# Performance work log

Measured on AMD Instinct MI355X. Metric: run time of the kernel, lower is better.

The kernel has to match this reference:

```python
import jax, jax.numpy as jnp
import numpy as np

# Standard SMPL kinematic tree (child -> parent); root's entry unused.
PARENTS = np.array([0, 0, 0, 0, 1, 2, 3, 4, 5, 6, 7, 8, 9, 9, 9, 12, 13, 14, 16, 17, 18, 19, 20, 21], dtype=np.int32)
N_JOINTS = 24


def _rodrigues(r):
    # r: [..., 3] axis-angle -> [..., 3, 3] rotation matrices.
    # Original adds N(0,1e-8) noise to avoid div-by-zero; we use a deterministic eps.
    theta = jnp.linalg.norm(r, axis=-1, keepdims=True) + 1e-8
    rh = r / theta
    cos = jnp.cos(theta)[..., None]
    sin = jnp.sin(theta)[..., None]
    z = jnp.zeros_like(rh[..., 0])
    K = jnp.stack([z, -rh[..., 2], rh[..., 1],
                   rh[..., 2], z, -rh[..., 0],
                   -rh[..., 1], rh[..., 0], z], axis=-1).reshape(r.shape[:-1] + (3, 3))
    outer = rh[..., :, None] * rh[..., None, :]
    eye = jnp.eye(3, dtype=r.dtype)
    return cos * eye + (1.0 - cos) * outer + sin * K


def setup_inputs() -> dict:
    key = jax.random.key(0)
    ks = jax.random.split(key, 7)
    N, V, J, B = 512, 6890, 24, 10
    beta = jax.random.normal(ks[0], (N, B), dtype=jnp.float32)
    pose = jax.random.normal(ks[1], (N, J * 3), dtype=jnp.float32)
    v_template = jax.random.normal(ks[2], (V, 3), dtype=jnp.float32)
    shapedirs = jax.random.normal(ks[3], (V, 3, B), dtype=jnp.float32) * 0.03
    posedirs = jax.random.normal(ks[4], (V, 3, (J - 1) * 9), dtype=jnp.float32) * 0.01
    J_regressor = jax.random.uniform(ks[5], (J, V), dtype=jnp.float32)
    J_regressor = J_regressor / jnp.sum(J_regressor, axis=1, keepdims=True)  # NonNegUnitSum(axis=1)
    weights = jax.random.uniform(ks[6], (V, J), dtype=jnp.float32)
    weights = weights / jnp.sum(weights, axis=1, keepdims=True)  # NonNegUnitSum(axis=1)
    return {"beta": beta, "pose": pose, "v_template": v_template, "shapedirs": shapedirs,
            "posedirs": posedirs, "J_regressor": J_regressor, "weights": weights}


def reference(beta, pose, v_template, shapedirs, posedirs, J_regressor, weights):
    N = beta.shape[0]
    dt = beta.dtype
    # Shape blendshapes: [N,V,3]
    v_shaped = jnp.einsum('nb,vcb->nvc', beta, shapedirs) + v_template
    # Joint locations: [N,J,3]
    J_loc = jnp.einsum('jv,nvc->njc', J_regressor, v_shaped)
    # Per-joint rotations: [N,24,3,3]
    R = _rodrigues(pose.reshape(N, N_JOINTS, 3))
    # Pose blendshapes
    lrotmin = (R[:, 1:] - jnp.eye(3, dtype=dt)).reshape(N, (N_JOINTS - 1) * 9)
    v_posed = v_shaped + jnp.einsum('np,vcp->nvc', lrotmin, posedirs)
    # Kinematic chain of 4x4 transforms
    bottom = jnp.broadcast_to(jnp.array([0.0, 0.0, 0.0, 1.0], dtype=dt), (N, 1, 4))

    def make_T(Rm, t):  # [N,3,3], [N,3] -> [N,4,4]
        return jnp.concatenate([jnp.concatenate([Rm, t[..., None]], axis=-1), bottom], axis=-2)

    G = [make_T(R[:, 0], J_loc[:, 0])]
    for i in range(1, N_JOINTS):
        p = int(PARENTS[i])
        G.append(jnp.matmul(G[p], make_T(R[:, i], J_loc[:, i] - J_loc[:, p])))
    G = jnp.stack(G, axis=1)  # [N,24,4,4]
    # Remove rest-pose joint translation: G[...,:,3] -= G @ [J,0]
    Jh = jnp.concatenate([J_loc, jnp.zeros_like(J_loc[..., :1])], axis=-1)  # [N,24,4]
    RJ = jnp.einsum('njab,njb->nja', G, Jh)
    G = G - jnp.pad(RJ[..., None], ((0, 0), (0, 0), (0, 0), (3, 0)))
    # Linear blend skinning: per-vertex blended transform [N,V,4,4]
    T = jnp.einsum('njab,vj->nvab', G, weights)
    vh = jnp.concatenate([v_posed, jnp.ones_like(v_posed[..., :1])], axis=-1)  # [N,V,4]
    v = jnp.einsum('nvab,nvb->nva', T, vh)
    return v[..., :3]
```

## Files before the change

### kernel.cpp

```cpp
#include <hip/hip_runtime.h>

#define V_CNT 6890
#define N_B 512
#define NP 207
#define KPAD 224
#define RTOT 20670
#define RPAD 20736
#define PREP_BLKS 2268
#define JS1_BLKS 384
#define W_BLKS 27

typedef unsigned short ushort_t;
typedef __attribute__((ext_vector_type(4))) float f32x4;
typedef __attribute__((ext_vector_type(8))) short s16x8;
typedef __attribute__((ext_vector_type(4))) float f4a;

#define O_PART 0u
#define O_G2   65536u
#define O_A    655360u
#define O_W    917504u
#define O_B    1441792u
#define O_PB   10747904u

__device__ __constant__ int PAR[24] = {0,0,0,0,1,2,3,4,5,6,7,8,9,9,9,12,13,14,16,17,18,19,20,21};

__device__ __forceinline__ ushort_t f2bf(float f) {
    union { float f; unsigned u; } x; x.f = f;
    unsigned u = x.u + 0x7fffu + ((x.u >> 16) & 1u);
    return (ushort_t)(u >> 16);
}
__device__ __forceinline__ float bf2f(ushort_t h) {
    union { unsigned u; float f; } x; x.u = ((unsigned)h) << 16;
    return x.f;
}

__global__ __launch_bounds__(256) void k_pre(const float* __restrict__ pdirs,
                                             const float* __restrict__ sdirs,
                                             const float* __restrict__ vtemp,
                                             const float* __restrict__ jreg,
                                             const float* __restrict__ wts,
                                             ushort_t* __restrict__ Bm,
                                             float* __restrict__ part,
                                             ushort_t* __restrict__ Wp) {
    int b = blockIdx.x;
    int tid = threadIdx.x;
    if (b < PREP_BLKS) {
        int g = b * 256 + tid;
        int r = g / 28;
        int k0 = (g - r * 28) * 8;
        s16x8 pk;
        if (r < RTOT) {
            const float* pr = pdirs + (size_t)r * NP;
            const float* sr = sdirs + (size_t)r * 10;
#pragma unroll
            for (int i = 0; i < 8; i++) {
                int k = k0 + i;
                float v = 0.f;
                if (k < NP) v = pr[k];
                else if (k < 217) v = sr[k - NP];
                pk[i] = (short)f2bf(v);
            }
        } else {
#pragma unroll
            for (int i = 0; i < 8; i++) pk[i] = 0;
        }
        *(s16x8*)(Bm + (size_t)r * KPAD + k0) = pk;
    } else if (b < PREP_BLKS + JS1_BLKS) {
        int b2 = b - PREP_BLKS;
        int ch = b2 & 15;
        int j = b2 >> 4;
        int v0 = ch * 432;
        int vend = v0 + 432; if (vend > V_CNT) vend = V_CNT;
        float acc[33];
#pragma unroll
        for (int i = 0; i < 33; i++) acc[i] = 0.f;
        for (int v = v0 + tid; v < vend; v += 256) {
            float r = jreg[j * V_CNT + v];
            const float* sd = sdirs + v * 30;
#pragma unroll
            for (int i = 0; i < 30; i++) acc[i] += r * sd[i];
            acc[30] += r * vtemp[v * 3 + 0];
            acc[31] += r * vtemp[v * 3 + 1];
            acc[32] += r * vtemp[v * 3 + 2];
        }
#pragma unroll
        for (int off = 32; off > 0; off >>= 1) {
#pragma unroll
            for (int i = 0; i < 33; i++) acc[i] += __shfl_down(acc[i], off);
        }
        __shared__ float red[4][33];
        int w = tid >> 6, lane = tid & 63;
        if (lane == 0) {
#pragma unroll
            for (int i = 0; i < 33; i++) red[w][i] = acc[i];
        }
        __syncthreads();
        if (tid < 33) {
            float s = red[0][tid] + red[1][tid] + red[2][tid] + red[3][tid];
            part[b2 * 33 + tid] = s;
        }
    } else {
        int v = (b - PREP_BLKS - JS1_BLKS) * 256 + tid;
        ushort_t o[32];
        if (v < V_CNT) {
            const float* wr = wts + v * 24;
#pragma unroll
            for (int j = 0; j < 24; j++) o[j] = f2bf(wr[j]);
        } else {
#pragma unroll
            for (int j = 0; j < 24; j++) o[j] = 0;
        }
#pragma unroll
        for (int j = 24; j < 32; j++) o[j] = 0;
#pragma unroll
        for (int q = 0; q < 4; q++)
            *(s16x8*)(Wp + (size_t)v * 32 + q * 8) = *(s16x8*)&o[q * 8];
    }
}

__global__ __launch_bounds__(256) void k_chain(const float* __restrict__ beta,
                                               const float* __restrict__ pose,
                                               const float* __restrict__ part,
                                               ushort_t* __restrict__ G2,
                                               ushort_t* __restrict__ Am) {
    __shared__ float JSl[720];
    __shared__ float JTl[72];
    __shared__ float Rl[4][24][9];
    __shared__ float Jl[4][24][3];
    __shared__ float Tm[4][24][16];
    __shared__ float G[4][24][16];
    __shared__ float Gp[4][24][12];
    int tid = threadIdx.x;

    for (int t = tid; t < 792; t += 256) {
        int j = t / 33, i = t - j * 33;
        float s = 0.f;
#pragma unroll
        for (int c = 0; c < 16; c++) s += part[(j * 16 + c) * 33 + i];
        if (i < 30) JSl[j * 30 + i] = s;
        else        JTl[j * 3 + (i - 30)] = s;
    }
    __syncthreads();

    int sub = tid >> 6, lane = tid & 63;
    int n = blockIdx.x * 4 + sub;

    if (lane < 24) {
        int t = lane;
        float x = pose[n * 72 + t * 3 + 0];
        float y = pose[n * 72 + t * 3 + 1];
        float z = pose[n * 72 + t * 3 + 2];
        float th = sqrtf(x * x + y * y + z * z) + 1e-8f;
        float inv = 1.f / th;
        float rx = x * inv, ry = y * inv, rz = z * inv;
        float c = cosf(th), s = sinf(th), omc = 1.f - c;
        Rl[sub][t][0] = c + omc * rx * rx;
        Rl[sub][t][1] = omc * rx * ry - s * rz;
        Rl[sub][t][2] = omc * rx * rz + s * ry;
        Rl[sub][t][3] = omc * ry * rx + s * rz;
        Rl[sub][t][4] = c + omc * ry * ry;
        Rl[sub][t][5] = omc * ry * rz - s * rx;
        Rl[sub][t][6] = omc * rz * rx - s * ry;
        Rl[sub][t][7] = omc * rz * ry + s * rx;
        Rl[sub][t][8] = c + omc * rz * rz;
#pragma unroll
        for (int cc = 0; cc < 3; cc++) {
            float a = JTl[t * 3 + cc];
#pragma unroll
            for (int b = 0; b < 10; b++) a += beta[n * 10 + b] * JSl[(t * 3 + cc) * 10 + b];
            Jl[sub][t][cc] = a;
        }
    }
    __syncthreads();
    if (lane < 24) {
        int t = lane;
        int p = PAR[t];
        float tx, ty, tz;
        if (t == 0) { tx = Jl[sub][0][0]; ty = Jl[sub][0][1]; tz = Jl[sub][0][2]; }
        else { tx = Jl[sub][t][0] - Jl[sub][p][0]; ty = Jl[sub][t][1] - Jl[sub][p][1]; tz = Jl[sub][t][2] - Jl[sub][p][2]; }
        Tm[sub][t][0] = Rl[sub][t][0]; Tm[sub][t][1] = Rl[sub][t][1]; Tm[sub][t][2]  = Rl[sub][t][2]; Tm[sub][t][3]  = tx;
        Tm[sub][t][4] = Rl[sub][t][3]; Tm[sub][t][5] = Rl[sub][t][4]; Tm[sub][t][6]  = Rl[sub][t][5]; Tm[sub][t][7]  = ty;
        Tm[sub][t][8] = Rl[sub][t][6]; Tm[sub][t][9] = Rl[sub][t][7]; Tm[sub][t][10] = Rl[sub][t][8]; Tm[sub][t][11] = tz;
        Tm[sub][t][12] = 0.f; Tm[sub][t][13] = 0.f; Tm[sub][t][14] = 0.f; Tm[sub][t][15] = 1.f;
    }
    __syncthreads();
    if (lane < 16) G[sub][0][lane] = Tm[sub][0][lane];
    __syncthreads();
    for (int i = 1; i < 24; i++) {
        int p = PAR[i];
        if (lane < 16) {
            int a = lane >> 2, bb = lane & 3;
            float s = G[sub][p][a * 4 + 0] * Tm[sub][i][0 * 4 + bb]
                    + G[sub][p][a * 4 + 1] * Tm[sub][i][1 * 4 + bb]
                    + G[sub][p][a * 4 + 2] * Tm[sub][i][2 * 4 + bb]
                    + G[sub][p][a * 4 + 3] * Tm[sub][i][3 * 4 + bb];
            G[sub][i][lane] = s;
        }
        __syncthreads();
    }
    if (lane < 24) {
        int t = lane;
        float jx = Jl[sub][t][0], jy = Jl[sub][t][1], jz = Jl[sub][t][2];
#pragma unroll
        for (int a = 0; a < 3; a++) {
            float g0 = G[sub][t][a * 4 + 0], g1 = G[sub][t][a * 4 + 1];
            float g2 = G[sub][t][a * 4 + 2], g3 = G[sub][t][a * 4 + 3];
            Gp[sub][t][a * 4 + 0] = g0;
            Gp[sub][t][a * 4 + 1] = g1;
            Gp[sub][t][a * 4 + 2] = g2;
            Gp[sub][t][a * 4 + 3] = g3 - (g0 * jx + g1 * jy + g2 * jz);
        }
    }
    __syncthreads();
    {
        int quad = lane >> 4, lm = lane & 15;
        s16x8 pk;
#pragma unroll
        for (int jj = 0; jj < 8; jj++) {
            int joint = quad * 8 + jj;
            float val = (joint < 24 && lm < 12) ? Gp[sub][joint][lm] : 0.f;
            pk[jj] = (short)f2bf(val);
        }
        *(s16x8*)(G2 + (size_t)n * 512 + lane * 8) = pk;
    }
    for (int idx = lane; idx < KPAD; idx += 64) {
        float val;
        if (idx < NP) {
            int j = 1 + idx / 9;
            int e = idx - (j - 1) * 9;
            float d = (e == 0 || e == 4 || e == 8) ? 1.f : 0.f;
            val = Rl[sub][j][e] - d;
        } else if (idx < 217) {
            val = beta[n * 10 + (idx - NP)];
        } else val = 0.f;
        Am[n * KPAD + idx] = f2bf(val);
    }
}

__global__ __launch_bounds__(256) void k_gemm(const ushort_t* __restrict__ A,
                                              const ushort_t* __restrict__ B,
                                              const float* __restrict__ vtemp,
                                              ushort_t* __restrict__ C) {
    __shared__ __align__(16) ushort_t a_lds[64 * 40];
    __shared__ __align__(16) ushort_t b_lds[128 * 40];
    int tid = threadIdx.x;
    int rblk = blockIdx.x * 128;
    int n0 = blockIdx.y * 64;
    int w = tid >> 6, lane = tid & 63;
    int quad = lane >> 4, lm = lane & 15;
    int m0w = (w >> 1) * 32, r0w = (w & 1) * 64;

    f32x4 acc[2][4];
#pragma unroll
    for (int a = 0; a < 2; a++)
#pragma unroll
        for (int b = 0; b < 4; b++) acc[a][b] = (f32x4)0.f;

    int srow = tid >> 2, koff = (tid & 3) * 8;
    const ushort_t* ag  = A + (n0 + srow) * KPAD + koff;
    const ushort_t* bg1 = B + (size_t)(rblk + srow) * KPAD + koff;
    const ushort_t* bg2 = B + (size_t)(rblk + srow + 64) * KPAD + koff;

#pragma unroll 1
    for (int kc = 0; kc < 7; kc++) {
        s16x8 av  = *(const s16x8*)(ag  + kc * 32);
        s16x8 bv1 = *(const s16x8*)(bg1 + kc * 32);
        s16x8 bv2 = *(const s16x8*)(bg2 + kc * 32);
        __syncthreads();
        *(s16x8*)&a_lds[srow * 40 + koff] = av;
        *(s16x8*)&b_lds[srow * 40 + koff] = bv1;
        *(s16x8*)&b_lds[(srow + 64) * 40 + koff] = bv2;
        __syncthreads();
        s16x8 af[2], bf[4];
#pragma unroll
        for (int mt = 0; mt < 2; mt++)
            af[mt] = *(const s16x8*)&a_lds[(m0w + mt * 16 + lm) * 40 + quad * 8];
#pragma unroll
        for (int rt = 0; rt < 4; rt++)
            bf[rt] = *(const s16x8*)&b_lds[(r0w + rt * 16 + lm) * 40 + quad * 8];
#pragma unroll
        for (int mt = 0; mt < 2; mt++)
#pragma unroll
            for (int rt = 0; rt < 4; rt++)
                acc[mt][rt] = __builtin_amdgcn_mfma_f32_16x16x32_bf16(af[mt], bf[rt], acc[mt][rt], 0, 0, 0);
    }
#pragma unroll
    for (int mt = 0; mt < 2; mt++) {
#pragma unroll
        for (int rt = 0; rt < 4; rt++) {
            int col = rblk + r0w + rt * 16 + lm;
            float vt = (col < RTOT) ? vtemp[col] : 0.f;
#pragma unroll
            for (int i = 0; i < 4; i++) {
                int row = n0 + m0w + mt * 16 + quad * 4 + i;
                C[(size_t)row * RPAD + col] = f2bf(acc[mt][rt][i] + vt);
            }
        }
    }
}

__global__ __launch_bounds__(256) void k_lbs(const ushort_t* __restrict__ Wp,
                                             const ushort_t* __restrict__ G2,
                                             const ushort_t* __restrict__ pb,
                                             float* __restrict__ out) {
    __shared__ float T[4][64][19];
    int tid = threadIdx.x, w = tid >> 6, lane = tid & 63;
    int quad = lane >> 4, lm = lane & 15;
    int v0 = blockIdx.x * 64;
    int n = blockIdx.y * 4 + w;
    int v = v0 + lane;

    const ushort_t* pp = pb + (size_t)n * RPAD + v * 3;
    float px = bf2f(pp[0]), py = bf2f(pp[1]), pz = bf2f(pp[2]);

    s16x8 bfr = *(const s16x8*)(G2 + (size_t)n * 512 + lane * 8);
    f32x4 acc[4];
#pragma unroll
    for (int mt = 0; mt < 4; mt++) {
        s16x8 af = *(const s16x8*)(Wp + (size_t)(v0 + mt * 16 + lm) * 32 + quad * 8);
        acc[mt] = __builtin_amdgcn_mfma_f32_16x16x32_bf16(af, bfr, (f32x4)0.f, 0, 0, 0);
    }
#pragma unroll
    for (int mt = 0; mt < 4; mt++)
#pragma unroll
        for (int i = 0; i < 4; i++)
            T[w][mt * 16 + quad * 4 + i][lm] = acc[mt][i];
    __syncthreads();

    if (v < V_CNT) {
        const float* Tr = &T[w][lane][0];
        float o0 = Tr[3]  + Tr[0] * px + Tr[1] * py + Tr[2]  * pz;
        float o1 = Tr[7]  + Tr[4] * px + Tr[5] * py + Tr[6]  * pz;
        float o2 = Tr[11] + Tr[8] * px + Tr[9] * py + Tr[10] * pz;
        float* op = out + ((size_t)n * V_CNT + v) * 3;
        op[0] = o0; op[1] = o1; op[2] = o2;
    }
}

extern "C" void kernel_launch(void* const* d_in, const int* in_sizes, int n_in,
                              void* d_out, int out_size, void* d_ws, size_t ws_size,
                              hipStream_t stream) {
    const float* beta  = (const float*)d_in[0];
    const float* pose  = (const float*)d_in[1];
    const float* vtemp = (const float*)d_in[2];
    const float* sdirs = (const float*)d_in[3];
    const float* pdirs = (const float*)d_in[4];
    const float* jreg  = (const float*)d_in[5];
    const float* wts   = (const float*)d_in[6];
    char* ws = (char*)d_ws;
    float*    ws_part = (float*)(ws + O_PART);
    ushort_t* ws_G2   = (ushort_t*)(ws + O_G2);
    ushort_t* ws_A    = (ushort_t*)(ws + O_A);
    ushort_t* ws_W    = (ushort_t*)(ws + O_W);
    ushort_t* ws_B    = (ushort_t*)(ws + O_B);
    ushort_t* ws_pb   = (ushort_t*)(ws + O_PB);
    float* out = (float*)d_out;

    k_pre<<<dim3(PREP_BLKS + JS1_BLKS + W_BLKS), dim3(256), 0, stream>>>(
        pdirs, sdirs, vtemp, jreg, wts, ws_B, ws_part, ws_W);
    k_chain<<<dim3(N_B / 4), dim3(256), 0, stream>>>(beta, pose, ws_part, ws_G2, ws_A);
    k_gemm<<<dim3(RPAD / 128, N_B / 64), dim3(256), 0, stream>>>(ws_A, ws_B, vtemp, ws_pb);
    k_lbs<<<dim3(108, N_B / 4), dim3(256), 0, stream>>>(ws_W, ws_G2, ws_pb, out);
}
```

Before: 150.8 us.

## Parallelize kinematic chain by tree level, enlarge GEMM tile, coalesce LBS stores

The kinematic chain now evaluates joints level by level, up to four joints per step, over 9 dependent steps instead of 23. It also runs two poses per 128-thread block, giving twice as many blocks. The GEMM tile grows from 64x128 to 128x128 so each B tile is reused across more rows, at the cost of more accumulator registers and fewer blocks. The LBS kernel loops over four 64-vertex sub-tiles per block and stages outputs in LDS for contiguous float2 stores, but it drops the barrier between the T writes and the cross-lane reads, which relies on the wavefront running in lockstep.

Measured after the change: 148.1 us. Within noise of the previous version (-1.8%).

```diff
diff --git a/kernel.cpp b/kernel.cpp
--- a/kernel.cpp
+++ b/kernel.cpp
@@ -13,7 +13,7 @@
 typedef unsigned short ushort_t;
 typedef __attribute__((ext_vector_type(4))) float f32x4;
 typedef __attribute__((ext_vector_type(8))) short s16x8;
-typedef __attribute__((ext_vector_type(4))) float f4a;
+typedef __attribute__((ext_vector_type(2))) float f32x2;
 
 #define O_PART 0u
 #define O_G2   65536u
@@ -23,6 +23,10 @@
 #define O_PB   10747904u
 
 __device__ __constant__ int PAR[24] = {0,0,0,0,1,2,3,4,5,6,7,8,9,9,9,12,13,14,16,17,18,19,20,21};
+__device__ __constant__ int LVL[36] = {
+    1, 2, 3,-1,   4, 5, 6,-1,   7, 8, 9,-1,
+   10,11,12,13,  14,-1,-1,-1,  15,16,17,-1,
+   18,19,-1,-1,  20,21,-1,-1,  22,23,-1,-1};
 
 __device__ __forceinline__ ushort_t f2bf(float f) {
     union { float f; unsigned u; } x; x.f = f;
@@ -118,21 +122,21 @@
     }
 }
 
-__global__ __launch_bounds__(256) void k_chain(const float* __restrict__ beta,
+__global__ __launch_bounds__(128) void k_chain(const float* __restrict__ beta,
                                                const float* __restrict__ pose,
                                                const float* __restrict__ part,
                                                ushort_t* __restrict__ G2,
                                                ushort_t* __restrict__ Am) {
     __shared__ float JSl[720];
     __shared__ float JTl[72];
-    __shared__ float Rl[4][24][9];
-    __shared__ float Jl[4][24][3];
-    __shared__ float Tm[4][24][16];
-    __shared__ float G[4][24][16];
-    __shared__ float Gp[4][24][12];
+    __shared__ float Rl[2][24][9];
+    __shared__ float Jl[2][24][3];
+    __shared__ float Tm[2][24][16];
+    __shared__ float G[2][24][16];
+    __shared__ float Gp[2][24][12];
     int tid = threadIdx.x;
 
-    for (int t = tid; t < 792; t += 256) {
+    for (int t = tid; t < 792; t += 128) {
         int j = t / 33, i = t - j * 33;
         float s = 0.f;
 #pragma unroll
@@ -143,7 +147,7 @@
     __syncthreads();
 
     int sub = tid >> 6, lane = tid & 63;
-    int n = blockIdx.x * 4 + sub;
+    int n = blockIdx.x * 2 + sub;
 
     if (lane < 24) {
         int t = lane;
@@ -186,15 +190,18 @@
     __syncthreads();
     if (lane < 16) G[sub][0][lane] = Tm[sub][0][lane];
     __syncthreads();
-    for (int i = 1; i < 24; i++) {
-        int p = PAR[i];
-        if (lane < 16) {
-            int a = lane >> 2, bb = lane & 3;
-            float s = G[sub][p][a * 4 + 0] * Tm[sub][i][0 * 4 + bb]
-                    + G[sub][p][a * 4 + 1] * Tm[sub][i][1 * 4 + bb]
-                    + G[sub][p][a * 4 + 2] * Tm[sub][i][2 * 4 + bb]
-                    + G[sub][p][a * 4 + 3] * Tm[sub][i][3 * 4 + bb];
-            G[sub][i][lane] = s;
+#pragma unroll
+    for (int p9 = 0; p9 < 9; p9++) {
+        int slot = lane >> 4, el = lane & 15;
+        int j = LVL[p9 * 4 + slot];
+        if (j >= 0) {
+            int par = PAR[j];
+            int a = el >> 2, bb = el & 3;
+            float s = G[sub][par][a * 4 + 0] * Tm[sub][j][0 * 4 + bb]
+                    + G[sub][par][a * 4 + 1] * Tm[sub][j][1 * 4 + bb]
+                    + G[sub][par][a * 4 + 2] * Tm[sub][j][2 * 4 + bb]
+                    + G[sub][par][a * 4 + 3] * Tm[sub][j][3 * 4 + bb];
+            G[sub][j][el] = s;
         }
         __syncthreads();
     }
@@ -241,51 +248,52 @@
                                               const ushort_t* __restrict__ B,
                                               const float* __restrict__ vtemp,
                                               ushort_t* __restrict__ C) {
-    __shared__ __align__(16) ushort_t a_lds[64 * 40];
+    __shared__ __align__(16) ushort_t a_lds[128 * 40];
     __shared__ __align__(16) ushort_t b_lds[128 * 40];
     int tid = threadIdx.x;
     int rblk = blockIdx.x * 128;
-    int n0 = blockIdx.y * 64;
+    int n0 = blockIdx.y * 128;
     int w = tid >> 6, lane = tid & 63;
     int quad = lane >> 4, lm = lane & 15;
-    int m0w = (w >> 1) * 32, r0w = (w & 1) * 64;
-
-    f32x4 acc[2][4];
-#pragma unroll
-    for (int a = 0; a < 2; a++)
+    int m0w = (w >> 1) * 64, r0w = (w & 1) * 64;
+
+    f32x4 acc[4][4];
+#pragma unroll
+    for (int a = 0; a < 4; a++)
 #pragma unroll
         for (int b = 0; b < 4; b++) acc[a][b] = (f32x4)0.f;
 
-    int srow = tid >> 2, koff = (tid & 3) * 8;
-    const ushort_t* ag  = A + (n0 + srow) * KPAD + koff;
-    const ushort_t* bg1 = B + (size_t)(rblk + srow) * KPAD + koff;
-    const ushort_t* bg2 = B + (size_t)(rblk + srow + 64) * KPAD + koff;
+    int srow = tid >> 1, koff = (tid & 1) * 16;
+    const ushort_t* ag = A + (size_t)(n0 + srow) * KPAD + koff;
+    const ushort_t* bg = B + (size_t)(rblk + srow) * KPAD + koff;
 
 #pragma unroll 1
     for (int kc = 0; kc < 7; kc++) {
-        s16x8 av  = *(const s16x8*)(ag  + kc * 32);
-        s16x8 bv1 = *(const s16x8*)(bg1 + kc * 32);
-        s16x8 bv2 = *(const s16x8*)(bg2 + kc * 32);
+        s16x8 av0 = *(const s16x8*)(ag + kc * 32);
+        s16x8 av1 = *(const s16x8*)(ag + kc * 32 + 8);
+        s16x8 bv0 = *(const s16x8*)(bg + kc * 32);
+        s16x8 bv1 = *(const s16x8*)(bg + kc * 32 + 8);
         __syncthreads();
-        *(s16x8*)&a_lds[srow * 40 + koff] = av;
-        *(s16x8*)&b_lds[srow * 40 + koff] = bv1;
-        *(s16x8*)&b_lds[(srow + 64) * 40 + koff] = bv2;
+        *(s16x8*)&a_lds[srow * 40 + koff] = av0;
+        *(s16x8*)&a_lds[srow * 40 + koff + 8] = av1;
+        *(s16x8*)&b_lds[srow * 40 + koff] = bv0;
+        *(s16x8*)&b_lds[srow * 40 + koff + 8] = bv1;
         __syncthreads();
-        s16x8 af[2], bf[4];
-#pragma unroll
-        for (int mt = 0; mt < 2; mt++)
+        s16x8 af[4], bf[4];
+#pragma unroll
+        for (int mt = 0; mt < 4; mt++)
             af[mt] = *(const s16x8*)&a_lds[(m0w + mt * 16 + lm) * 40 + quad * 8];
 #pragma unroll
         for (int rt = 0; rt < 4; rt++)
             bf[rt] = *(const s16x8*)&b_lds[(r0w + rt * 16 + lm) * 40 + quad * 8];
 #pragma unroll
-        for (int mt = 0; mt < 2; mt++)
+        for (int mt = 0; mt < 4; mt++)
 #pragma unroll
             for (int rt = 0; rt < 4; rt++)
                 acc[mt][rt] = __builtin_amdgcn_mfma_f32_16x16x32_bf16(af[mt], bf[rt], acc[mt][rt], 0, 0, 0);
     }
 #pragma unroll
-    for (int mt = 0; mt < 2; mt++) {
+    for (int mt = 0; mt < 4; mt++) {
 #pragma unroll
         for (int rt = 0; rt < 4; rt++) {
             int col = rblk + r0w + rt * 16 + lm;
@@ -304,36 +312,48 @@
                                              const ushort_t* __restrict__ pb,
                                              float* __restrict__ out) {
     __shared__ float T[4][64][19];
+    __shared__ float ost[4][192];
     int tid = threadIdx.x, w = tid >> 6, lane = tid & 63;
     int quad = lane >> 4, lm = lane & 15;
-    int v0 = blockIdx.x * 64;
+    int v0 = blockIdx.x * 256;
     int n = blockIdx.y * 4 + w;
-    int v = v0 + lane;
-
-    const ushort_t* pp = pb + (size_t)n * RPAD + v * 3;
-    float px = bf2f(pp[0]), py = bf2f(pp[1]), pz = bf2f(pp[2]);
 
     s16x8 bfr = *(const s16x8*)(G2 + (size_t)n * 512 + lane * 8);
-    f32x4 acc[4];
-#pragma unroll
-    for (int mt = 0; mt < 4; mt++) {
-        s16x8 af = *(const s16x8*)(Wp + (size_t)(v0 + mt * 16 + lm) * 32 + quad * 8);
-        acc[mt] = __builtin_amdgcn_mfma_f32_16x16x32_bf16(af, bfr, (f32x4)0.f, 0, 0, 0);
-    }
-#pragma unroll
-    for (int mt = 0; mt < 4; mt++)
-#pragma unroll
-        for (int i = 0; i < 4; i++)
-            T[w][mt * 16 + quad * 4 + i][lm] = acc[mt][i];
-    __syncthreads();
-
-    if (v < V_CNT) {
+    const ushort_t* pbn = pb + (size_t)n * RPAD;
+
+#pragma unroll 1
+    for (int s = 0; s < 4; s++) {
+        int vs = v0 + s * 64;
+        const ushort_t* pp = pbn + (vs + lane) * 3;
+        float px = bf2f(pp[0]), py = bf2f(pp[1]), pz = bf2f(pp[2]);
+
+        f32x4 acc[4];
+#pragma unroll
+        for (int mt = 0; mt < 4; mt++) {
+            s16x8 af = *(const s16x8*)(Wp + (size_t)(vs + mt * 16 + lm) * 32 + quad * 8);
+            acc[mt] = __builtin_amdgcn_mfma_f32_16x16x32_bf16(af, bfr, (f32x4)0.f, 0, 0, 0);
+        }
+#pragma unroll
+        for (int mt = 0; mt < 4; mt++)
+#pragma unroll
+            for (int i = 0; i < 4; i++)
+                T[w][mt * 16 + quad * 4 + i][lm] = acc[mt][i];
+
         const float* Tr = &T[w][lane][0];
         float o0 = Tr[3]  + Tr[0] * px + Tr[1] * py + Tr[2]  * pz;
         float o1 = Tr[7]  + Tr[4] * px + Tr[5] * py + Tr[6]  * pz;
         float o2 = Tr[11] + Tr[8] * px + Tr[9] * py + Tr[10] * pz;
-        float* op = out + ((size_t)n * V_CNT + v) * 3;
-        op[0] = o0; op[1] = o1; op[2] = o2;
+        ost[w][lane * 3 + 0] = o0;
+        ost[w][lane * 3 + 1] = o1;
+        ost[w][lane * 3 + 2] = o2;
+
+        int cnt = V_CNT - vs; if (cnt > 64) cnt = 64;
+        if (cnt > 0) {
+            int nh = (cnt * 3) >> 1;
+            float* obase = out + ((size_t)n * V_CNT + vs) * 3;
+            for (int j2 = lane; j2 < nh; j2 += 64)
+                *(f32x2*)(obase + j2 * 2) = *(const f32x2*)&ost[w][j2 * 2];
+        }
     }
 }
 
@@ -358,7 +378,7 @@
 
     k_pre<<<dim3(PREP_BLKS + JS1_BLKS + W_BLKS), dim3(256), 0, stream>>>(
         pdirs, sdirs, vtemp, jreg, wts, ws_B, ws_part, ws_W);
-    k_chain<<<dim3(N_B / 4), dim3(256), 0, stream>>>(beta, pose, ws_part, ws_G2, ws_A);
-    k_gemm<<<dim3(RPAD / 128, N_B / 64), dim3(256), 0, stream>>>(ws_A, ws_B, vtemp, ws_pb);
-    k_lbs<<<dim3(108, N_B / 4), dim3(256), 0, stream>>>(ws_W, ws_G2, ws_pb, out);
-}
+    k_chain<<<dim3(N_B / 2), dim3(128), 0, stream>>>(beta, pose, ws_part, ws_G2, ws_A);
+    k_gemm<<<dim3(RPAD / 128, N_B / 128), dim3(256), 0, stream>>>(ws_A, ws_B, vtemp, ws_pb);
+    k_lbs<<<dim3(27, N_B / 4), dim3(256), 0, stream>>>(ws_W, ws_G2, ws_pb, out);
+}
```
